# Kernel optimization log

Measured on AMD Instinct MI355X. Metric: run time of the kernel, lower is better.

The kernel has to match this reference:

```python
import jax, jax.numpy as jnp
import numpy as np

B, S, E, H = 2, 2048, 1024, 16
DH = E // H


def setup_inputs() -> dict:
    key = jax.random.key(0)
    ks = jax.random.split(key, 8)
    scale = 1.0 / np.sqrt(E)
    return {
        "in_feats": jax.random.normal(ks[0], (B, S, E), jnp.float32),
        "mul_encs": jax.random.normal(ks[1], (B, S, E), jnp.float32),
        "add_encs": jax.random.normal(ks[2], (B, S, E), jnp.float32),
        "ln_w": jnp.ones((E,), jnp.float32),
        "ln_b": jnp.zeros((E,), jnp.float32),
        "in_proj_w": jax.random.uniform(ks[3], (3 * E, E), jnp.float32, -scale, scale),
        "in_proj_b": jnp.zeros((3 * E,), jnp.float32),
        "out_proj_w": jax.random.uniform(ks[4], (E, E), jnp.float32, -scale, scale),
        "out_proj_b": jnp.zeros((E,), jnp.float32),
    }


def _layernorm(x, w, b, eps=1e-5):
    mu = jnp.mean(x, axis=-1, keepdims=True)
    var = jnp.var(x, axis=-1, keepdims=True)
    return (x - mu) * jax.lax.rsqrt(var + eps) * w + b


def reference(in_feats, mul_encs, add_encs, ln_w, ln_b, in_proj_w, in_proj_b, out_proj_w, out_proj_b):
    # norm + act pre-processing (torch nn.GELU default = exact erf gelu)
    d = _layernorm(in_feats, ln_w, ln_b)
    d = jax.nn.gelu(d, approximate=False)
    values = d
    qk_in = d * mul_encs + add_encs  # QK encoding modulation

    wq, wk, wv = jnp.split(in_proj_w, 3, axis=0)
    bq, bk, bv = jnp.split(in_proj_b, 3, axis=0)
    q = (qk_in @ wq.T + bq).reshape(B, S, H, DH)
    k = (qk_in @ wk.T + bk).reshape(B, S, H, DH)
    v = (values @ wv.T + bv).reshape(B, S, H, DH)

    scale = 1.0 / np.sqrt(DH)
    scores = jnp.einsum("bqhd,bkhd->bhqk", q * scale, k)  # [B,H,S,S]
    attn = jax.nn.softmax(scores, axis=-1)
    out = jnp.einsum("bhqk,bkhd->bqhd", attn, v).reshape(B, S, E)
    out = out @ out_proj_w.T + out_proj_b
    return in_feats + out  # skip connection
```

## Files before the change

### kernel.cpp

```cpp
#include <hip/hip_runtime.h>
#include <stdint.h>


typedef __attribute__((ext_vector_type(8))) short bf16x8;
typedef __attribute__((ext_vector_type(4))) short bf16x4;
typedef __attribute__((ext_vector_type(4))) float f32x4;
typedef __attribute__((ext_vector_type(4))) unsigned short u16x4;

#define DEV __device__ __forceinline__

DEV unsigned short f2bf(float f) {
  uint32_t u = __float_as_uint(f);
  u += 0x7fff + ((u >> 16) & 1);
  return (unsigned short)(u >> 16);
}

DEV float fast_exp2(float x) {
#if __has_builtin(__builtin_amdgcn_exp2f)
  return __builtin_amdgcn_exp2f(x);
#else
  return exp2f(x);
#endif
}

DEV f32x4 mfma16x16x16_bf16(bf16x4 a, bf16x4 b, f32x4 c) {
#if __has_builtin(__builtin_amdgcn_mfma_f32_16x16x16bf16_1k)
  return __builtin_amdgcn_mfma_f32_16x16x16bf16_1k(a, b, c, 0, 0, 0);
#else
  asm("v_mfma_f32_16x16x16_bf16 %0, %1, %2, %0" : "+v"(c) : "v"(a), "v"(b));
  return c;
#endif
}

DEV void gload_lds16(const void* g, void* l) {
  __builtin_amdgcn_global_load_lds(
      (const __attribute__((address_space(1))) uint32_t*)g,
      (__attribute__((address_space(3))) uint32_t*)l, 16, 0, 0);
}

__global__ __launch_bounds__(256) void wconv(const float* w1, const float* w2,
                                             unsigned short* o1, unsigned short* o2) {
  int i = blockIdx.x * 256 + threadIdx.x;
  const int n1 = 3145728 / 4;
  f32x4 v;
  if (i < n1) v = ((const f32x4*)w1)[i];
  else        v = ((const f32x4*)w2)[i - n1];
  u16x4 r;
#pragma unroll
  for (int j = 0; j < 4; ++j) r[j] = f2bf(v[j]);
  if (i < n1) ((u16x4*)o1)[i] = r;
  else        ((u16x4*)o2)[i - n1] = r;
}

__global__ __launch_bounds__(256) void preproc(const float* x, const float* mul, const float* add,
                                               const float* lw, const float* lb,
                                               unsigned short* values, unsigned short* qkin) {
  int row = blockIdx.x;
  size_t base = (size_t)row * 1024;
  int t = threadIdx.x;
  f32x4 v = ((const f32x4*)(x + base))[t];
  float s  = v[0] + v[1] + v[2] + v[3];
  float s2 = v[0]*v[0] + v[1]*v[1] + v[2]*v[2] + v[3]*v[3];
#pragma unroll
  for (int off = 1; off < 64; off <<= 1) {
    s  += __shfl_xor(s, off);
    s2 += __shfl_xor(s2, off);
  }
  __shared__ float rs[4], rs2[4];
  if ((t & 63) == 0) { rs[t >> 6] = s; rs2[t >> 6] = s2; }
  __syncthreads();
  s  = rs[0] + rs[1] + rs[2] + rs[3];
  s2 = rs2[0] + rs2[1] + rs2[2] + rs2[3];
  float mean = s * 0.0009765625f;
  float var  = s2 * 0.0009765625f - mean * mean;
  float rstd = rsqrtf(var + 1e-5f);
  f32x4 mu = ((const f32x4*)(mul + base))[t];
  f32x4 ad = ((const f32x4*)(add + base))[t];
  f32x4 w4 = ((const f32x4*)lw)[t];
  f32x4 b4 = ((const f32x4*)lb)[t];
  u16x4 vo, qo;
#pragma unroll
  for (int i = 0; i < 4; ++i) {
    float d = (v[i] - mean) * rstd * w4[i] + b4[i];
    float g = 0.5f * d * (1.0f + erff(d * 0.70710678118f));
    vo[i] = f2bf(g);
    qo[i] = f2bf(g * mu[i] + ad[i]);
  }
  ((u16x4*)(values + base))[t] = vo;
  ((u16x4*)(qkin   + base))[t] = qo;
}

DEV void gemm_tile(const unsigned short* A, const unsigned short* B, int K,
                   int m0, int n0, unsigned short* ldsA, unsigned short* ldsB,
                   f32x4 acc[4][4]) {
  int t = threadIdx.x;
  int lane = t & 63;
  int w = t >> 6;
  int wr = w >> 1, wc = w & 1;
  int l15 = lane & 15, l4 = lane >> 4;
  for (int k0 = 0; k0 < K; k0 += 64) {
#pragma unroll
    for (int i = 0; i < 4; ++i) {
      int idx = i * 256 + t;
      int r = idx >> 3;
      int slot = (idx & 7) ^ (r & 7);
      gload_lds16(A + (size_t)(m0 + r) * K + k0 + slot * 8,
                  (char*)ldsA + i * 4096 + w * 1024);
      gload_lds16(B + (size_t)(n0 + r) * K + k0 + slot * 8,
                  (char*)ldsB + i * 4096 + w * 1024);
    }
    __syncthreads();
#pragma unroll
    for (int kk = 0; kk < 2; ++kk) {
      bf16x8 af[4], bfr[4];
      int kb = kk * 64 + l4 * 16;
#pragma unroll
      for (int mm = 0; mm < 4; ++mm) {
        int r = wr * 64 + mm * 16 + l15;
        af[mm] = *(const bf16x8*)((const char*)ldsA + r * 128 + (kb ^ ((r & 7) << 4)));
      }
#pragma unroll
      for (int nn = 0; nn < 4; ++nn) {
        int r = wc * 64 + nn * 16 + l15;
        bfr[nn] = *(const bf16x8*)((const char*)ldsB + r * 128 + (kb ^ ((r & 7) << 4)));
      }
#pragma unroll
      for (int mm = 0; mm < 4; ++mm)
#pragma unroll
        for (int nn = 0; nn < 4; ++nn)
          acc[mm][nn] = __builtin_amdgcn_mfma_f32_16x16x32_bf16(af[mm], bfr[nn], acc[mm][nn], 0, 0, 0);
    }
    __syncthreads();
  }
}

#define QSCALE 0.18033688011112042f

__global__ __launch_bounds__(256) void gemm_qkv(const unsigned short* Aqk, const unsigned short* Av,
                                                const unsigned short* W, const float* bias,
                                                unsigned short* qws, unsigned short* kws,
                                                unsigned short* vtws) {
  __shared__ unsigned short lds[2 * 128 * 64];
  unsigned short* ldsA = lds;
  unsigned short* ldsB = lds + 128 * 64;
  int n0 = blockIdx.x * 128;
  int m0 = blockIdx.y * 128;
  const unsigned short* A = (n0 < 2048) ? Aqk : Av;
  f32x4 z = {0.f, 0.f, 0.f, 0.f};
  f32x4 acc[4][4];
#pragma unroll
  for (int mm = 0; mm < 4; ++mm)
#pragma unroll
    for (int nn = 0; nn < 4; ++nn) acc[mm][nn] = z;
  gemm_tile(A, W, 1024, m0, n0, ldsA, ldsB, acc);

  int t = threadIdx.x, lane = t & 63, w = t >> 6;
  int wr = w >> 1, wc = w & 1;
  int l15 = lane & 15, l4 = lane >> 4;
  int region = n0 >> 10;
  int bb = m0 >> 11, s0 = m0 & 2047;

  if (region == 2) {
    __syncthreads();
#pragma unroll
    for (int mm = 0; mm < 4; ++mm) {
#pragma unroll
      for (int nn = 0; nn < 4; ++nn) {
        int col = wc * 64 + nn * 16 + l15;
        float bs = bias[n0 + col];
#pragma unroll
        for (int reg = 0; reg < 4; ++reg) {
          int row = wr * 64 + mm * 16 + l4 * 4 + reg;
          *(unsigned short*)((char*)lds + row * 256 + ((col * 2) ^ ((row & 7) << 4))) =
              f2bf(acc[mm][nn][reg] + bs);
        }
      }
    }
    __syncthreads();
    int c = t >> 1, hl = t & 1;
    int e0 = n0 - 2048;
    int h = (e0 + c) >> 6, d = (e0 + c) & 63;
    unsigned short* dst = vtws + ((size_t)(bb * 16 + h) * 64 + d) * 2048 + s0 + hl * 64;
#pragma unroll
    for (int j0 = 0; j0 < 64; j0 += 8) {
      bf16x8 pk;
#pragma unroll
      for (int j = 0; j < 8; ++j) {
        int s = hl * 64 + j0 + j;
        pk[j] = *(const short*)((const char*)lds + s * 256 + ((c * 2) ^ ((s & 7) << 4)));
      }
      *(bf16x8*)(dst + j0) = pk;
    }
  } else {
    unsigned short* dst0 = region == 0 ? qws : kws;
    float scl = region == 0 ? QSCALE : 1.0f;
#pragma unroll
    for (int mm = 0; mm < 4; ++mm) {
      int row0 = m0 + wr * 64 + mm * 16 + l4 * 4;
      int sr = row0 & 2047;
#pragma unroll
      for (int nn = 0; nn < 4; ++nn) {
        int col = n0 + wc * 64 + nn * 16 + l15;
        float bs = bias[col];
        int e = col & 1023;
        int h = e >> 6, d = e & 63;
#pragma unroll
        for (int reg = 0; reg < 4; ++reg)
          dst0[(((size_t)(bb * 16 + h)) * 2048 + sr + reg) * 64 + d] = f2bf((acc[mm][nn][reg] + bs) * scl);
      }
    }
  }
}

DEV void stage_k(const unsigned short* Kp, int kv0, unsigned short* buf, int t) {
  int w = t >> 6;
#pragma unroll
  for (int i = 0; i < 2; ++i) {
    int idx = i * 256 + t;
    int r = idx >> 3;
    int slot = (idx & 7) ^ (r & 7);
    gload_lds16(Kp + (size_t)(kv0 + r) * 64 + slot * 8,
                (char*)buf + i * 4096 + w * 1024);
  }
}

DEV void stage_vt(const unsigned short* Vt, int kv0, unsigned short* buf, int t) {
  int w = t >> 6;
#pragma unroll
  for (int i = 0; i < 2; ++i) {
    int idx = i * 256 + t;
    int r = idx >> 3;
    int slot = (idx & 7) ^ (r & 7);
    gload_lds16(Vt + (size_t)r * 2048 + kv0 + slot * 8,
                (char*)buf + i * 4096 + w * 1024);
  }
}

DEV void attn_compute(const unsigned short* kbuf, const unsigned short* vtbuf,
                      const bf16x8 (&aq)[2][2], f32x4 (&o)[2][4],
                      float (&m_run)[2], float (&l_run)[2], const int (&osrc)[4],
                      int l15, int l4) {
  f32x4 z = {0.f, 0.f, 0.f, 0.f};
  f32x4 sc[2][4];
#pragma unroll
  for (int qs = 0; qs < 2; ++qs)
#pragma unroll
    for (int nn = 0; nn < 4; ++nn) sc[qs][nn] = z;
  __builtin_amdgcn_s_setprio(1);
#pragma unroll
  for (int kk = 0; kk < 2; ++kk) {
#pragma unroll
    for (int nn = 0; nn < 4; ++nn) {
      int r = nn * 16 + l15;
      bf16x8 bk = *(const bf16x8*)((const char*)kbuf + r * 128 + ((kk * 64 + l4 * 16) ^ ((r & 7) << 4)));
#pragma unroll
      for (int qs = 0; qs < 2; ++qs)
        sc[qs][nn] = __builtin_amdgcn_mfma_f32_16x16x32_bf16(bk, aq[qs][kk], sc[qs][nn], 0, 0, 0);
    }
  }
  __builtin_amdgcn_s_setprio(0);

  bf16x4 pa[2][4];
  float pmax[2];
#pragma unroll
  for (int qs = 0; qs < 2; ++qs) {
    float mA = fmaxf(fmaxf(sc[qs][0][0], sc[qs][0][1]), fmaxf(sc[qs][0][2], sc[qs][0][3]));
    float mB = fmaxf(fmaxf(sc[qs][1][0], sc[qs][1][1]), fmaxf(sc[qs][1][2], sc[qs][1][3]));
    float mC = fmaxf(fmaxf(sc[qs][2][0], sc[qs][2][1]), fmaxf(sc[qs][2][2], sc[qs][2][3]));
    float mD = fmaxf(fmaxf(sc[qs][3][0], sc[qs][3][1]), fmaxf(sc[qs][3][2], sc[qs][3][3]));
    float pm = fmaxf(fmaxf(mA, mB), fmaxf(mC, mD));
    pm = fmaxf(pm, __shfl_xor(pm, 16));
    pm = fmaxf(pm, __shfl_xor(pm, 32));
    pmax[qs] = pm;
  }

  if (__any(fmaxf(pmax[0] - m_run[0], pmax[1] - m_run[1]) > 8.0f)) {
#pragma unroll
    for (int qs = 0; qs < 2; ++qs) {
      float mnew = fmaxf(m_run[qs], pmax[qs]);
      float fs = fast_exp2(m_run[qs] - mnew);
      m_run[qs] = mnew;
      l_run[qs] *= fs;
      float fo[4];
#pragma unroll
      for (int reg = 0; reg < 4; ++reg) fo[reg] = __shfl(fs, osrc[reg]);
#pragma unroll
      for (int dt = 0; dt < 4; ++dt)
#pragma unroll
        for (int reg = 0; reg < 4; ++reg) o[qs][dt][reg] *= fo[reg];
    }
  }

#pragma unroll
  for (int qs = 0; qs < 2; ++qs) {
    float psum = 0.f;
#pragma unroll
    for (int nn = 0; nn < 4; ++nn) {
      float p0 = fast_exp2(sc[qs][nn][0] - m_run[qs]);
      float p1 = fast_exp2(sc[qs][nn][1] - m_run[qs]);
      float p2 = fast_exp2(sc[qs][nn][2] - m_run[qs]);
      float p3 = fast_exp2(sc[qs][nn][3] - m_run[qs]);
      psum += (p0 + p1) + (p2 + p3);
      pa[qs][nn][0] = (short)(__float_as_uint(p0) >> 16);
      pa[qs][nn][1] = (short)(__float_as_uint(p1) >> 16);
      pa[qs][nn][2] = (short)(__float_as_uint(p2) >> 16);
      pa[qs][nn][3] = (short)(__float_as_uint(p3) >> 16);
    }
    psum += __shfl_xor(psum, 16);
    psum += __shfl_xor(psum, 32);
    l_run[qs] += psum;
  }

  __builtin_amdgcn_s_setprio(1);
#pragma unroll
  for (int dt = 0; dt < 4; ++dt) {
    int r = dt * 16 + l15;
#pragma unroll
    for (int nn = 0; nn < 4; ++nn) {
      bf16x4 vb = *(const bf16x4*)((const char*)vtbuf + r * 128 + ((nn * 32 + l4 * 8) ^ ((r & 7) << 4)));
#pragma unroll
      for (int qs = 0; qs < 2; ++qs)
        o[qs][dt] = mfma16x16x16_bf16(pa[qs][nn], vb, o[qs][dt]);
    }
  }
  __builtin_amdgcn_s_setprio(0);
}

__global__ __launch_bounds__(256, 4) void attn_kernel(const unsigned short* qws, const unsigned short* kws,
                                                      const unsigned short* vtws,
                                                      unsigned short* po0, unsigned short* po1,
                                                      float* stats) {
  int qt = blockIdx.x;
  int bh = blockIdx.y;
  int half = blockIdx.z;
  int q0 = qt * 128;
  int kvbase = half * 1024;
  int t = threadIdx.x;
  int lane = t & 63, w = t >> 6;
  int l15 = lane & 15, l4 = lane >> 4;
  __shared__ unsigned short ldsK[2][64 * 64];
  __shared__ unsigned short ldsVT[2][64 * 64];

  const unsigned short* Qp = qws + ((size_t)bh * 2048 + q0 + w * 32) * 64;
  const unsigned short* Kp = kws + ((size_t)bh * 2048 + kvbase) * 64;
  const unsigned short* Vt = vtws + (size_t)bh * 64 * 2048 + kvbase;

  bf16x8 aq[2][2];
#pragma unroll
  for (int qs = 0; qs < 2; ++qs)
#pragma unroll
    for (int kk = 0; kk < 2; ++kk)
      aq[qs][kk] = *(const bf16x8*)(Qp + (qs * 16 + l15) * 64 + kk * 32 + l4 * 8);

  f32x4 z = {0.f, 0.f, 0.f, 0.f};
  f32x4 o[2][4];
#pragma unroll
  for (int qs = 0; qs < 2; ++qs)
#pragma unroll
    for (int i = 0; i < 4; ++i) o[qs][i] = z;
  float m_run[2] = {-1e30f, -1e30f};
  float l_run[2] = {0.f, 0.f};

  int osrc[4];
#pragma unroll
  for (int reg = 0; reg < 4; ++reg)
    osrc[reg] = (lane & 48) | (((lane >> 4) & 3) << 2) | reg;

  stage_k(Kp, 0, &ldsK[0][0], t);
  stage_vt(Vt, 0, &ldsVT[0][0], t);
  __syncthreads();

  for (int it = 0; it < 16; ++it) {
    int cur = it & 1;
    if (it < 15) {
      stage_k(Kp, (it + 1) * 64, &ldsK[cur ^ 1][0], t);
      stage_vt(Vt, (it + 1) * 64, &ldsVT[cur ^ 1][0], t);
    }
    attn_compute(&ldsK[cur][0], &ldsVT[cur][0], aq, o, m_run, l_run, osrc, l15, l4);
    __syncthreads();
  }

  unsigned short* po = half ? po1 : po0;
#pragma unroll
  for (int qs = 0; qs < 2; ++qs) {
#pragma unroll
    for (int reg = 0; reg < 4; ++reg) {
      int qg = q0 + w * 32 + qs * 16 + l4 * 4 + reg;
#pragma unroll
      for (int dt = 0; dt < 4; ++dt) {
        int d = dt * 16 + l15;
        po[((size_t)bh * 2048 + qg) * 64 + d] = f2bf(o[qs][dt][reg]);
      }
    }
  }
  if (l4 == 0) {
#pragma unroll
    for (int qs = 0; qs < 2; ++qs) {
      int qg = q0 + w * 32 + qs * 16 + l15;
      size_t si = (((size_t)half * 32 + bh) * 2048 + qg) * 2;
      stats[si] = m_run[qs];
      stats[si + 1] = l_run[qs];
    }
  }
}

__global__ __launch_bounds__(256) void attn_merge(const unsigned short* po0, const unsigned short* po1,
                                                  const float* stats, unsigned short* attnb) {
  int row = blockIdx.x;
  int b = row >> 11, q = row & 2047;
  int t = threadIdx.x;
  int c0 = t * 4;
  int h = c0 >> 6, d = c0 & 63;
  int bh = b * 16 + h;
  size_t si0 = ((size_t)bh * 2048 + q) * 2;
  size_t si1 = (((size_t)32 + bh) * 2048 + q) * 2;
  float m0 = stats[si0], l0 = stats[si0 + 1];
  float m1 = stats[si1], l1 = stats[si1 + 1];
  float m = fmaxf(m0, m1);
  float f0 = fast_exp2(m0 - m), f1 = fast_exp2(m1 - m);
  float inv = 1.0f / (l0 * f0 + l1 * f1);
  float a0 = f0 * inv, a1 = f1 * inv;
  size_t off = ((size_t)bh * 2048 + q) * 64 + d;
  u16x4 x0 = *(const u16x4*)(po0 + off);
  u16x4 x1 = *(const u16x4*)(po1 + off);
  u16x4 r;
#pragma unroll
  for (int j = 0; j < 4; ++j) {
    float v0 = __uint_as_float((uint32_t)x0[j] << 16);
    float v1 = __uint_as_float((uint32_t)x1[j] << 16);
    r[j] = f2bf(v0 * a0 + v1 * a1);
  }
  *(u16x4*)(attnb + (size_t)row * 1024 + c0) = r;
}

__global__ __launch_bounds__(256) void gemm_out(const unsigned short* A, const unsigned short* W,
                                                const float* bias, const float* resid, float* out) {
  __shared__ unsigned short ldsA[128 * 64];
  __shared__ unsigned short ldsB[64 * 64];
  int n0 = blockIdx.x * 64;
  int m0 = blockIdx.y * 128;
  int t = threadIdx.x;
  int lane = t & 63;
  int w = t >> 6;
  int l15 = lane & 15, l4 = lane >> 4;
  f32x4 z = {0.f, 0.f, 0.f, 0.f};
  f32x4 acc[2][4];
#pragma unroll
  for (int mm = 0; mm < 2; ++mm)
#pragma unroll
    for (int nn = 0; nn < 4; ++nn) acc[mm][nn] = z;

  for (int k0 = 0; k0 < 1024; k0 += 64) {
#pragma unroll
    for (int i = 0; i < 4; ++i) {
      int idx = i * 256 + t;
      int r = idx >> 3;
      int slot = (idx & 7) ^ (r & 7);
      gload_lds16(A + (size_t)(m0 + r) * 1024 + k0 + slot * 8,
                  (char*)ldsA + i * 4096 + w * 1024);
    }
#pragma unroll
    for (int i = 0; i < 2; ++i) {
      int idx = i * 256 + t;
      int r = idx >> 3;
      int slot = (idx & 7) ^ (r & 7);
      gload_lds16(W + (size_t)(n0 + r) * 1024 + k0 + slot * 8,
                  (char*)ldsB + i * 4096 + w * 1024);
    }
    __syncthreads();
#pragma unroll
    for (int kk = 0; kk < 2; ++kk) {
      bf16x8 af[2], bfr[4];
      int kb = kk * 64 + l4 * 16;
#pragma unroll
      for (int mm = 0; mm < 2; ++mm) {
        int r = w * 32 + mm * 16 + l15;
        af[mm] = *(const bf16x8*)((const char*)ldsA + r * 128 + (kb ^ ((r & 7) << 4)));
      }
#pragma unroll
      for (int nn = 0; nn < 4; ++nn) {
        int r = nn * 16 + l15;
        bfr[nn] = *(const bf16x8*)((const char*)ldsB + r * 128 + (kb ^ ((r & 7) << 4)));
      }
#pragma unroll
      for (int mm = 0; mm < 2; ++mm)
#pragma unroll
        for (int nn = 0; nn < 4; ++nn)
          acc[mm][nn] = __builtin_amdgcn_mfma_f32_16x16x32_bf16(af[mm], bfr[nn], acc[mm][nn], 0, 0, 0);
    }
    __syncthreads();
  }

#pragma unroll
  for (int mm = 0; mm < 2; ++mm) {
#pragma unroll
    for (int nn = 0; nn < 4; ++nn) {
      int col = n0 + nn * 16 + l15;
      float bs = bias[col];
#pragma unroll
      for (int reg = 0; reg < 4; ++reg) {
        int r = m0 + w * 32 + mm * 16 + l4 * 4 + reg;
        size_t off = (size_t)r * 1024 + col;
        out[off] = acc[mm][nn][reg] + bs + resid[off];
      }
    }
  }
}

extern "C" void kernel_launch(void* const* d_in, const int* in_sizes, int n_in,
                              void* d_out, int out_size, void* d_ws, size_t ws_size,
                              hipStream_t stream) {
  const float* in_feats   = (const float*)d_in[0];
  const float* mul_encs   = (const float*)d_in[1];
  const float* add_encs   = (const float*)d_in[2];
  const float* ln_w       = (const float*)d_in[3];
  const float* ln_b       = (const float*)d_in[4];
  const float* in_proj_w  = (const float*)d_in[5];
  const float* in_proj_b  = (const float*)d_in[6];
  const float* out_proj_w = (const float*)d_in[7];
  const float* out_proj_b = (const float*)d_in[8];
  float* out = (float*)d_out;

  unsigned short* ws = (unsigned short*)d_ws;
  unsigned short* values = ws;
  unsigned short* qkin   = values + 4194304;
  unsigned short* wqkv   = qkin + 4194304;
  unsigned short* wout   = wqkv + 3145728;
  unsigned short* qws    = wout + 1048576;
  unsigned short* kws    = qws + 4194304;
  unsigned short* vtws   = kws + 4194304;
  unsigned short* attnb  = vtws + 4194304;

  unsigned short* po0   = values;
  unsigned short* po1   = qkin;
  float*          stats = (float*)wqkv;

  wconv<<<4096, 256, 0, stream>>>(in_proj_w, out_proj_w, wqkv, wout);
  preproc<<<4096, 256, 0, stream>>>(in_feats, mul_encs, add_encs, ln_w, ln_b, values, qkin);
  gemm_qkv<<<dim3(24, 32), 256, 0, stream>>>(qkin, values, wqkv, in_proj_b, qws, kws, vtws);
  attn_kernel<<<dim3(16, 32, 2), 256, 0, stream>>>(qws, kws, vtws, po0, po1, stats);
  attn_merge<<<4096, 256, 0, stream>>>(po0, po1, stats, attnb);
  gemm_out<<<dim3(16, 32), 256, 0, stream>>>(attnb, wout, out_proj_b, in_feats, out);
}
```

Before: 152.5 us.

## Load K fragments directly into registers instead of staging through LDS

Result: slower. 215.8 us (+41.5%).

```diff
diff --git a/kernel.cpp b/kernel.cpp
--- a/kernel.cpp
+++ b/kernel.cpp
@@ -212,16 +212,12 @@
   }
 }
 
-DEV void stage_k(const unsigned short* Kp, int kv0, unsigned short* buf, int t) {
-  int w = t >> 6;
-#pragma unroll
-  for (int i = 0; i < 2; ++i) {
-    int idx = i * 256 + t;
-    int r = idx >> 3;
-    int slot = (idx & 7) ^ (r & 7);
-    gload_lds16(Kp + (size_t)(kv0 + r) * 64 + slot * 8,
-                (char*)buf + i * 4096 + w * 1024);
-  }
+DEV void load_kfrag(const unsigned short* Kp, int kv0, int l15, int l4, bf16x8 (&kf)[8]) {
+#pragma unroll
+  for (int nn = 0; nn < 4; ++nn)
+#pragma unroll
+    for (int kk = 0; kk < 2; ++kk)
+      kf[nn * 2 + kk] = *(const bf16x8*)(Kp + (size_t)(kv0 + nn * 16 + l15) * 64 + kk * 32 + l4 * 8);
 }
 
 DEV void stage_vt(const unsigned short* Vt, int kv0, unsigned short* buf, int t) {
@@ -236,10 +232,11 @@
   }
 }
 
-DEV void attn_compute(const unsigned short* kbuf, const unsigned short* vtbuf,
-                      const bf16x8 (&aq)[2][2], f32x4 (&o)[2][4],
-                      float (&m_run)[2], float (&l_run)[2], const int (&osrc)[4],
-                      int l15, int l4) {
+DEV void attn_step(const bf16x8 (&kf)[8], const unsigned short* vtbuf,
+                   bool pre, const unsigned short* Kp, int kvn, bf16x8 (&kfn)[8],
+                   const bf16x8 (&aq)[2][2], f32x4 (&o)[2][4],
+                   float (&m_run)[2], float (&l_run)[2], const int (&osrc)[4],
+                   int l15, int l4) {
   f32x4 z = {0.f, 0.f, 0.f, 0.f};
   f32x4 sc[2][4];
 #pragma unroll
@@ -248,17 +245,15 @@
     for (int nn = 0; nn < 4; ++nn) sc[qs][nn] = z;
   __builtin_amdgcn_s_setprio(1);
 #pragma unroll
-  for (int kk = 0; kk < 2; ++kk) {
-#pragma unroll
-    for (int nn = 0; nn < 4; ++nn) {
-      int r = nn * 16 + l15;
-      bf16x8 bk = *(const bf16x8*)((const char*)kbuf + r * 128 + ((kk * 64 + l4 * 16) ^ ((r & 7) << 4)));
+  for (int kk = 0; kk < 2; ++kk)
+#pragma unroll
+    for (int nn = 0; nn < 4; ++nn)
 #pragma unroll
       for (int qs = 0; qs < 2; ++qs)
-        sc[qs][nn] = __builtin_amdgcn_mfma_f32_16x16x32_bf16(bk, aq[qs][kk], sc[qs][nn], 0, 0, 0);
-    }
-  }
+        sc[qs][nn] = __builtin_amdgcn_mfma_f32_16x16x32_bf16(kf[nn * 2 + kk], aq[qs][kk], sc[qs][nn], 0, 0, 0);
   __builtin_amdgcn_s_setprio(0);
+
+  if (pre) load_kfrag(Kp, kvn, l15, l4, kfn);
 
   bf16x4 pa[2][4];
   float pmax[2];
@@ -326,7 +321,7 @@
   __builtin_amdgcn_s_setprio(0);
 }
 
-__global__ __launch_bounds__(256, 4) void attn_kernel(const unsigned short* qws, const unsigned short* kws,
+__global__ __launch_bounds__(256, 3) void attn_kernel(const unsigned short* qws, const unsigned short* kws,
                                                       const unsigned short* vtws,
                                                       unsigned short* po0, unsigned short* po1,
                                                       float* stats) {
@@ -338,7 +333,6 @@
   int t = threadIdx.x;
   int lane = t & 63, w = t >> 6;
   int l15 = lane & 15, l4 = lane >> 4;
-  __shared__ unsigned short ldsK[2][64 * 64];
   __shared__ unsigned short ldsVT[2][64 * 64];
 
   const unsigned short* Qp = qws + ((size_t)bh * 2048 + q0 + w * 32) * 64;
@@ -366,17 +360,21 @@
   for (int reg = 0; reg < 4; ++reg)
     osrc[reg] = (lane & 48) | (((lane >> 4) & 3) << 2) | reg;
 
-  stage_k(Kp, 0, &ldsK[0][0], t);
+  bf16x8 kfA[8], kfB[8];
+
+  load_kfrag(Kp, 0, l15, l4, kfA);
   stage_vt(Vt, 0, &ldsVT[0][0], t);
   __syncthreads();
 
-  for (int it = 0; it < 16; ++it) {
-    int cur = it & 1;
-    if (it < 15) {
-      stage_k(Kp, (it + 1) * 64, &ldsK[cur ^ 1][0], t);
-      stage_vt(Vt, (it + 1) * 64, &ldsVT[cur ^ 1][0], t);
-    }
-    attn_compute(&ldsK[cur][0], &ldsVT[cur][0], aq, o, m_run, l_run, osrc, l15, l4);
+  for (int it = 0; it < 16; it += 2) {
+    stage_vt(Vt, (it + 1) * 64, &ldsVT[1][0], t);
+    attn_step(kfA, &ldsVT[0][0], true, Kp, (it + 1) * 64, kfB,
+              aq, o, m_run, l_run, osrc, l15, l4);
+    __syncthreads();
+    bool pre = (it + 2) < 16;
+    if (pre) stage_vt(Vt, (it + 2) * 64, &ldsVT[0][0], t);
+    attn_step(kfB, &ldsVT[1][0], pre, Kp, (it + 2) * 64, kfA,
+              aq, o, m_run, l_run, osrc, l15, l4);
     __syncthreads();
   }
 
```
